# Optimization experiments

Measured on AMD Instinct MI355X. Metric: run time of the kernel, lower is better.

## Reference

```python
import jax
import jax.numpy as jnp
import numpy as np
from jax import lax

# Butterworth order-2 lowpass, Wn=0.25 (scipy.signal.butter(2, 0.25))
_B = [0.0976310729378175, 0.195262145875635, 0.0976310729378175]
_A = [1.0, -0.9428090415820634, 0.33333333333333337]


def setup_inputs() -> dict:
    key = jax.random.key(0)
    x = jax.random.normal(key, (128, 8, 32768), dtype=jnp.float32)
    b = jnp.array(_B, dtype=jnp.float32)
    a = jnp.array(_A, dtype=jnp.float32)
    return {"x": x, "b": b, "a": a}


def _odd_ext(x, n):
    # scipy-style odd extension along the last axis
    left = 2.0 * x[..., :1] - x[..., 1:n + 1][..., ::-1]
    right = 2.0 * x[..., -1:] - x[..., -n - 1:-1][..., ::-1]
    return jnp.concatenate([left, x, right], axis=-1)


def _lfilter(b, a, x):
    # Direct-form II transposed IIR filter along last axis, zero initial state.
    b = b / a[0]
    a = a / a[0]
    order = b.shape[0] - 1  # static
    b_tail, a_tail = b[1:], a[1:]
    z0 = jnp.zeros(x.shape[:-1] + (order,), dtype=x.dtype)
    xT = jnp.moveaxis(x, -1, 0)  # [T, ...batch]

    def step(z, xt):
        yt = b[0] * xt + z[..., 0]
        z_shift = jnp.concatenate([z[..., 1:], jnp.zeros_like(z[..., :1])], axis=-1)
        z_new = z_shift + b_tail * xt[..., None] - a_tail * yt[..., None]
        return z_new, yt

    _, yT = lax.scan(step, z0, xT)
    return jnp.moveaxis(yT, 0, -1)


def _filtfilt(x, a, b):
    y = _lfilter(b, a, x)
    y = _lfilter(b, a, y[..., ::-1])
    return y[..., ::-1]


def reference(x, b, a):
    scale = jnp.max(jnp.abs(x), axis=-1, keepdims=True)
    xn = x / scale
    padlen = 3 * max(int(a.shape[0]), int(b.shape[0]))  # static = 9
    xe = _odd_ext(xn, padlen)
    y = _filtfilt(xe, a, b)
    y = y[..., padlen:-padlen]
    return y * scale
```

## Files before the change

### kernel.cpp

```cpp
#include <hip/hip_runtime.h>


#define N_COLS 32768
#define PAD 9
#define LTOT (N_COLS + 2 * PAD)
#define SEGS 4
#define S_OUT 8192
#define WF 24
#define WB 24
#define CF 34
#define CB 33
#define TPB 256
#define FB (WF + CF)
#define KB (CB + WB)
#define MAXSZ (CF * TPB + WF)

__launch_bounds__(TPB, 4)
__global__ void filtfilt_kernel(const float* __restrict__ x,
                                const float* __restrict__ bco,
                                const float* __restrict__ aco,
                                float* __restrict__ out) {
    __shared__ float xs[MAXSZ];
    const int seg = blockIdx.x;
    const int row = blockIdx.y;
    const int tid = threadIdx.x;

    const float inv_a0 = 1.0f / aco[0];
    const float B0 = bco[0] * inv_a0;
    const float B1 = bco[1] * inv_a0;
    const float B2 = bco[2] * inv_a0;
    const float A1 = aco[1] * inv_a0;
    const float A2 = aco[2] * inv_a0;

    const int G = PAD + seg * S_OUT;
    int A = G - WF; if (A < 0) A = 0;
    int B = G + CF * TPB; if (B > LTOT) B = LTOT;

    const float* __restrict__ xrow = x + (size_t)row * N_COLS;

    int gi0 = A - PAD; if (gi0 < 0) gi0 = 0;
    int gi1 = B - PAD; if (gi1 > N_COLS) gi1 = N_COLS;
    const int off0 = gi0 + PAD - A;
    const int nvec = (gi1 - gi0) >> 2;
    const float4* __restrict__ xg4 = (const float4*)(xrow + gi0);
    if (off0 == 0) {
        float4* xs4 = (float4*)xs;
        for (int i = tid; i < nvec; i += TPB) xs4[i] = xg4[i];
    } else {
        for (int i = tid; i < nvec; i += TPB) {
            float4 v = xg4[i];
            const int u = off0 + 4 * i;
            xs[u] = v.x; xs[u + 1] = v.y; xs[u + 2] = v.z; xs[u + 3] = v.w;
        }
    }
    for (int g = gi0 + 4 * nvec + tid; g < gi1; g += TPB)
        xs[off0 + (g - gi0)] = xrow[g];
    if (tid < PAD) {
        if (A == 0) {
            const int t = tid;
            xs[t] = 2.0f * xrow[0] - xrow[PAD - t];
        }
        if (B == LTOT) {
            const int t = N_COLS + PAD + tid;
            xs[t - A] = 2.0f * xrow[N_COLS - 1] - xrow[2 * N_COLS + PAD - 2 - t];
        }
    }
    __syncthreads();

    const int sf = G + CF * tid;
    float v[FB];
#pragma unroll
    for (int k = 0; k < FB; ++k) {
        const int t = sf - WF + k;
        v[k] = (t >= A) ? xs[t - A] : 0.0f;
    }
    {
        float z0 = 0.0f, z1 = 0.0f;
#pragma unroll
        for (int k = 0; k < FB; ++k) {
            const float xv = v[k];
            const float y = fmaf(B0, xv, z0);
            z0 = fmaf(-A1, y, fmaf(B1, xv, z1));
            z1 = fmaf(B2, xv, -A2 * y);
            v[k] = y;
        }
    }
    __syncthreads();
#pragma unroll
    for (int k = WF; k < FB; ++k) {
        const int t = sf + (k - WF);
        if (t < B) xs[t - A] = v[k];
    }
    __syncthreads();

    const int sb = G + CB * tid;
    float w[KB];
#pragma unroll
    for (int k = 0; k < KB; ++k) w[k] = xs[sb + k - A];
    {
        float z0 = 0.0f, z1 = 0.0f;
#pragma unroll
        for (int kk = KB - 1; kk >= 0; --kk) {
            const int t = sb + kk;
            if (t < LTOT) {
                const float xv = w[kk];
                const float y = fmaf(B0, xv, z0);
                z0 = fmaf(-A1, y, fmaf(B1, xv, z1));
                z1 = fmaf(B2, xv, -A2 * y);
                if (kk < CB) w[kk] = y;
            }
        }
    }
    __syncthreads();
#pragma unroll
    for (int k = 0; k < CB; ++k) {
        const int t = sb + k;
        if (t < B) xs[t - A] = w[k];
    }
    __syncthreads();

    float* __restrict__ orow = out + (size_t)row * N_COLS + (size_t)seg * S_OUT;
    const int off = G - A;
    if ((off & 3) == 0) {
        float4* o4 = (float4*)orow;
        const float4* s4 = (const float4*)(xs + off);
        for (int i = tid; i < S_OUT / 4; i += TPB) o4[i] = s4[i];
    } else {
        float4* o4 = (float4*)orow;
        for (int i = tid; i < S_OUT / 4; i += TPB) {
            const int u = off + 4 * i;
            float4 t;
            t.x = xs[u]; t.y = xs[u + 1]; t.z = xs[u + 2]; t.w = xs[u + 3];
            o4[i] = t;
        }
    }
}

extern "C" void kernel_launch(void* const* d_in, const int* in_sizes, int n_in,
                              void* d_out, int out_size, void* d_ws, size_t ws_size,
                              hipStream_t stream) {
    const float* x = (const float*)d_in[0];
    const float* b = (const float*)d_in[1];
    const float* a = (const float*)d_in[2];
    float* out = (float*)d_out;
    const int rows = out_size / N_COLS;
    dim3 grid(SEGS, rows);
    filtfilt_kernel<<<grid, TPB, 0, stream>>>(x, b, a, out);
}
```

Before: 250.3 us.

## Restructure filtfilt into independent per-wavefront segments without block barriers

Each row is now split into 31 segments, each handled by one 64-lane wavefront with its own LDS slot, in place of 4 segments per 256-thread block. Warm-up windows shrink from 24 to 16 samples and chunks per lane shrink, and all __syncthreads barriers go away because a wavefront works only on its own slot. Occupancy hint rises to 8 blocks. The aim is more parallel segments, less redundant warm-up work and no block-wide syncs, while relying on a shorter 16-sample transient approximation and on wavefront-synchronous LDS use without explicit barriers.

```diff
diff --git a/kernel.cpp b/kernel.cpp
--- a/kernel.cpp
+++ b/kernel.cpp
@@ -3,27 +3,35 @@
 
 #define N_COLS 32768
 #define PAD 9
-#define LTOT (N_COLS + 2 * PAD)
-#define SEGS 4
-#define S_OUT 8192
-#define WF 24
-#define WB 24
-#define CF 34
-#define CB 33
+#define LTOT  (N_COLS + 2 * PAD)
+#define OUTEND (N_COLS + PAD)
+#define WF 16
+#define WB 16
+#define CF 19
+#define CB 17
+#define LANES 64
+#define P   (CB * LANES)
+#define NSEG 31
+#define SLOT (WF + CF * LANES)
+#define WPB 4
 #define TPB 256
-#define FB (WF + CF)
-#define KB (CB + WB)
-#define MAXSZ (CF * TPB + WF)
 
-__launch_bounds__(TPB, 4)
+__launch_bounds__(TPB, 8)
 __global__ void filtfilt_kernel(const float* __restrict__ x,
                                 const float* __restrict__ bco,
                                 const float* __restrict__ aco,
-                                float* __restrict__ out) {
-    __shared__ float xs[MAXSZ];
-    const int seg = blockIdx.x;
-    const int row = blockIdx.y;
+                                float* __restrict__ out,
+                                int rows) {
+    __shared__ float xs_all[WPB][SLOT];
     const int tid = threadIdx.x;
+    const int wid = tid >> 6;
+    const int lane = tid & 63;
+    float* __restrict__ xs = xs_all[wid];
+
+    const int W = blockIdx.x * WPB + wid;
+    const int row = W / NSEG;
+    const int seg = W - row * NSEG;
+    if (row >= rows) return;
 
     const float inv_a0 = 1.0f / aco[0];
     const float B0 = bco[0] * inv_a0;
@@ -32,52 +40,42 @@
     const float A1 = aco[1] * inv_a0;
     const float A2 = aco[2] * inv_a0;
 
-    const int G = PAD + seg * S_OUT;
-    int A = G - WF; if (A < 0) A = 0;
-    int B = G + CF * TPB; if (B > LTOT) B = LTOT;
-
+    const int G = PAD + seg * P;
+    const int A = G - WF;
     const float* __restrict__ xrow = x + (size_t)row * N_COLS;
 
-    int gi0 = A - PAD; if (gi0 < 0) gi0 = 0;
-    int gi1 = B - PAD; if (gi1 > N_COLS) gi1 = N_COLS;
-    const int off0 = gi0 + PAD - A;
-    const int nvec = (gi1 - gi0) >> 2;
-    const float4* __restrict__ xg4 = (const float4*)(xrow + gi0);
-    if (off0 == 0) {
-        float4* xs4 = (float4*)xs;
-        for (int i = tid; i < nvec; i += TPB) xs4[i] = xg4[i];
-    } else {
-        for (int i = tid; i < nvec; i += TPB) {
-            float4 v = xg4[i];
-            const int u = off0 + 4 * i;
-            xs[u] = v.x; xs[u + 1] = v.y; xs[u + 2] = v.z; xs[u + 3] = v.w;
+    {
+        const int g0 = (A - PAD > 0) ? (A - PAD) : 0;
+        int g1 = G + CF * LANES; if (g1 > OUTEND) g1 = OUTEND; g1 -= PAD;
+        const int off0 = g0 + PAD - A;
+        const float4* __restrict__ xg4 = (const float4*)(xrow + g0);
+        float4* __restrict__ s4 = (float4*)(xs + off0);
+        const int nvec = (g1 - g0) >> 2;
+        for (int i = lane; i < nvec; i += LANES) s4[i] = xg4[i];
+    }
+    if (seg == 0) {
+        if (lane < WF) {
+            const int t = lane - (WF - PAD);
+            xs[lane] = (t >= 0) ? (2.0f * xrow[0] - xrow[PAD - t]) : 0.0f;
         }
     }
-    for (int g = gi0 + 4 * nvec + tid; g < gi1; g += TPB)
-        xs[off0 + (g - gi0)] = xrow[g];
-    if (tid < PAD) {
-        if (A == 0) {
-            const int t = tid;
-            xs[t] = 2.0f * xrow[0] - xrow[PAD - t];
-        }
-        if (B == LTOT) {
-            const int t = N_COLS + PAD + tid;
-            xs[t - A] = 2.0f * xrow[N_COLS - 1] - xrow[2 * N_COLS + PAD - 2 - t];
+    if (seg == NSEG - 1) {
+        const float x_last = xrow[N_COLS - 1];
+        for (int o = (OUTEND - A) + lane; o < SLOT; o += LANES) {
+            const int t = A + o;
+            xs[o] = (t < LTOT) ? (2.0f * x_last - xrow[2 * N_COLS + PAD - 2 - t])
+                               : 0.0f;
         }
     }
-    __syncthreads();
 
-    const int sf = G + CF * tid;
-    float v[FB];
+    const int f_off = CF * lane;
+    float v[WF + CF];
 #pragma unroll
-    for (int k = 0; k < FB; ++k) {
-        const int t = sf - WF + k;
-        v[k] = (t >= A) ? xs[t - A] : 0.0f;
-    }
+    for (int k = 0; k < WF + CF; ++k) v[k] = xs[f_off + k];
     {
         float z0 = 0.0f, z1 = 0.0f;
 #pragma unroll
-        for (int k = 0; k < FB; ++k) {
+        for (int k = 0; k < WF + CF; ++k) {
             const float xv = v[k];
             const float y = fmaf(B0, xv, z0);
             z0 = fmaf(-A1, y, fmaf(B1, xv, z1));
@@ -85,55 +83,37 @@
             v[k] = y;
         }
     }
-    __syncthreads();
 #pragma unroll
-    for (int k = WF; k < FB; ++k) {
-        const int t = sf + (k - WF);
-        if (t < B) xs[t - A] = v[k];
+    for (int k = WF; k < WF + CF; ++k) xs[f_off + k] = v[k];
+
+    if (seg == NSEG - 1) {
+        for (int o = (LTOT - A) + lane; o < SLOT; o += LANES) xs[o] = 0.0f;
     }
-    __syncthreads();
 
-    const int sb = G + CB * tid;
-    float w[KB];
+    const int b_off = CB * lane + WF;
+    float w[CB + WB];
 #pragma unroll
-    for (int k = 0; k < KB; ++k) w[k] = xs[sb + k - A];
+    for (int k = 0; k < CB + WB; ++k) w[k] = xs[b_off + k];
     {
         float z0 = 0.0f, z1 = 0.0f;
 #pragma unroll
-        for (int kk = KB - 1; kk >= 0; --kk) {
-            const int t = sb + kk;
-            if (t < LTOT) {
-                const float xv = w[kk];
-                const float y = fmaf(B0, xv, z0);
-                z0 = fmaf(-A1, y, fmaf(B1, xv, z1));
-                z1 = fmaf(B2, xv, -A2 * y);
-                if (kk < CB) w[kk] = y;
-            }
+        for (int k = CB + WB - 1; k >= 0; --k) {
+            const float xv = w[k];
+            const float y = fmaf(B0, xv, z0);
+            z0 = fmaf(-A1, y, fmaf(B1, xv, z1));
+            z1 = fmaf(B2, xv, -A2 * y);
+            if (k < CB) w[k] = y;
         }
     }
-    __syncthreads();
 #pragma unroll
-    for (int k = 0; k < CB; ++k) {
-        const int t = sb + k;
-        if (t < B) xs[t - A] = w[k];
-    }
-    __syncthreads();
+    for (int k = 0; k < CB; ++k) xs[b_off + k] = w[k];
 
-    float* __restrict__ orow = out + (size_t)row * N_COLS + (size_t)seg * S_OUT;
-    const int off = G - A;
-    if ((off & 3) == 0) {
-        float4* o4 = (float4*)orow;
-        const float4* s4 = (const float4*)(xs + off);
-        for (int i = tid; i < S_OUT / 4; i += TPB) o4[i] = s4[i];
-    } else {
-        float4* o4 = (float4*)orow;
-        for (int i = tid; i < S_OUT / 4; i += TPB) {
-            const int u = off + 4 * i;
-            float4 t;
-            t.x = xs[u]; t.y = xs[u + 1]; t.z = xs[u + 2]; t.w = xs[u + 3];
-            o4[i] = t;
-        }
-    }
+    int nout = OUTEND - G; if (nout > P) nout = P;
+    float* __restrict__ orow = out + (size_t)row * N_COLS + (G - PAD);
+    const float4* __restrict__ s4 = (const float4*)(xs + WF);
+    float4* __restrict__ o4 = (float4*)orow;
+    const int nv = nout >> 2;
+    for (int i = lane; i < nv; i += LANES) o4[i] = s4[i];
 }
 
 extern "C" void kernel_launch(void* const* d_in, const int* in_sizes, int n_in,
@@ -144,6 +124,7 @@
     const float* a = (const float*)d_in[2];
     float* out = (float*)d_out;
     const int rows = out_size / N_COLS;
-    dim3 grid(SEGS, rows);
-    filtfilt_kernel<<<grid, TPB, 0, stream>>>(x, b, a, out);
+    const int total_waves = rows * NSEG;
+    const int blocks = (total_waves + WPB - 1) / WPB;
+    filtfilt_kernel<<<blocks, TPB, 0, stream>>>(x, b, a, out, rows);
 }
```

New measurement: 240.7 us. 1.04x faster.
